# Performance work log

Hardware: AMD Instinct MI355X
Metric: run time of the kernel (lower is better)

Reference implementation:

```python
import jax, jax.numpy as jnp
import numpy as np

D_MODEL = 1024
N_HEADS = 16
HEAD_DIM = D_MODEL // N_HEADS


def _linear_params(key, fan_in, fan_out):
    kw, kb = jax.random.split(key)
    bound = 1.0 / np.sqrt(fan_in)
    W = jax.random.uniform(kw, (fan_in, fan_out), jnp.float32, -bound, bound)
    b = jax.random.uniform(kb, (fan_out,), jnp.float32, -bound, bound)
    return W, b


def setup_inputs() -> dict:
    key = jax.random.key(0)
    ks = jax.random.split(key, 7)
    B, N = 4, 2048
    q = jax.random.normal(ks[0], (B, N, D_MODEL), jnp.float32)
    k = jax.random.normal(ks[1], (B, N, D_MODEL), jnp.float32)
    v = jax.random.normal(ks[2], (B, N, D_MODEL), jnp.float32)
    Wq, bq = _linear_params(ks[3], D_MODEL, D_MODEL)
    Wk, bk = _linear_params(ks[4], D_MODEL, D_MODEL)
    Wv, bv = _linear_params(ks[5], D_MODEL, D_MODEL)
    Wo, bo = _linear_params(ks[6], D_MODEL, D_MODEL)
    return {"q": q, "k": k, "v": v,
            "Wq": Wq, "bq": bq, "Wk": Wk, "bk": bk,
            "Wv": Wv, "bv": bv, "Wo": Wo, "bo": bo}


def reference(q, k, v, Wq, bq, Wk, bk, Wv, bv, Wo, bo):
    B, N, _ = q.shape
    # fused QKV projection + head split: [B, N, D] -> [B, H, N, hd]
    def split_heads(x):
        return x.reshape(B, N, N_HEADS, HEAD_DIM).transpose(0, 2, 1, 3)
    qh = split_heads(q @ Wq + bq)
    kh = split_heads(k @ Wk + bk)
    vh = split_heads(v @ Wv + bv)
    # scaled dot-product attention (mask=None)
    scale = 1.0 / np.sqrt(HEAD_DIM)
    scores = jnp.einsum('bhqd,bhkd->bhqk', qh, kh) * scale  # [B,H,N,N]
    attn_weights = jax.nn.softmax(scores, axis=-1)
    attn_out = jnp.einsum('bhqk,bhkd->bhqd', attn_weights, vh)
    # merge heads: [B,H,N,hd] -> [B,N,D]
    attn_out = attn_out.transpose(0, 2, 1, 3).reshape(B, N, D_MODEL)
    output = attn_out @ Wo + bo
    return output, attn_weights
```

## Files before the change

### kernel.cpp

```cpp
#include <hip/hip_runtime.h>
#include <hip/hip_bf16.h>
#include <stdint.h>

#define D_MODEL 1024
#define NH      16
#define HD      64
#define B_SZ    4
#define SEQ     2048
#define M_TOT   (B_SZ*SEQ)
#define LOG2E_O8 0.18033688011112042f

typedef __bf16 bf16;
typedef bf16  bf16x8 __attribute__((ext_vector_type(8)));
typedef bf16  bf16x4 __attribute__((ext_vector_type(4)));
typedef float f32x4  __attribute__((ext_vector_type(4)));

static __device__ __forceinline__ f32x4 mfma16(bf16x8 a, bf16x8 b, f32x4 c) {
  return __builtin_amdgcn_mfma_f32_16x16x32_bf16(a, b, c, 0, 0, 0);
}

static __device__ __forceinline__ void gl2lds(const void* g, void* l) {
  __builtin_amdgcn_global_load_lds(
      (const __attribute__((address_space(1))) unsigned int*)g,
      (__attribute__((address_space(3))) unsigned int*)l,
      16, 0, 0);
}

#define BAR_VM16() do { \
  asm volatile("s_waitcnt vmcnt(16) lgkmcnt(0)" ::: "memory"); \
  __builtin_amdgcn_s_barrier(); \
  __builtin_amdgcn_sched_barrier(0); \
} while (0)

#define BAR_LGKM() do { \
  asm volatile("s_waitcnt lgkmcnt(0)" ::: "memory"); \
  __builtin_amdgcn_s_barrier(); \
  __builtin_amdgcn_sched_barrier(0); \
} while (0)

__global__ __launch_bounds__(256) void k_twt(const float* __restrict__ w0,
                                             const float* __restrict__ w1,
                                             const float* __restrict__ w2,
                                             const float* __restrict__ w3,
                                             bf16* __restrict__ t0,
                                             bf16* __restrict__ t1,
                                             bf16* __restrict__ t2,
                                             bf16* __restrict__ t3) {
  __shared__ bf16 t[64][65];
  int z = blockIdx.z;
  const float* W = z == 0 ? w0 : z == 1 ? w1 : z == 2 ? w2 : w3;
  bf16* Wt = z == 0 ? t0 : z == 1 ? t1 : z == 2 ? t2 : t3;
  int k0 = blockIdx.x * 64, n0 = blockIdx.y * 64;
  int r = threadIdx.x >> 2, c0 = (threadIdx.x & 3) * 16;
  const float* p = W + (size_t)(k0 + r) * D_MODEL + n0 + c0;
#pragma unroll
  for (int e = 0; e < 16; e += 4) {
    float4 v = *(const float4*)(p + e);
    t[r][c0+e+0] = (bf16)v.x; t[r][c0+e+1] = (bf16)v.y;
    t[r][c0+e+2] = (bf16)v.z; t[r][c0+e+3] = (bf16)v.w;
  }
  __syncthreads();
  bf16x8 o0, o1;
#pragma unroll
  for (int e = 0; e < 8; e++) { o0[e] = t[c0+e][r]; o1[e] = t[c0+8+e][r]; }
  bf16* q = Wt + (size_t)(n0 + r) * D_MODEL + k0 + c0;
  *(bf16x8*)q = o0; *(bf16x8*)(q + 8) = o1;
}

__global__ __launch_bounds__(256) void k_qkv(const float* __restrict__ Aq,
                                             const float* __restrict__ Ak,
                                             const float* __restrict__ Av,
                                             const bf16* __restrict__ Wt3,
                                             const float* __restrict__ bq,
                                             const float* __restrict__ bk,
                                             const float* __restrict__ bv,
                                             bf16* __restrict__ HQ,
                                             bf16* __restrict__ Vt) {
  __shared__ alignas(16) bf16 sA[2][8192];
  __shared__ alignas(16) bf16 sB[2][8192];
  const int tid = threadIdx.x;
  const int lane = tid & 63, wv = tid >> 6;
  const int g = lane >> 4, lr = lane & 15;
  const int wm = wv >> 1, wn = wv & 1;
  const int d = blockIdx.x;
  const int p = (d & 7) * 24 + (d >> 6);
  const int seg = p >> 6;
  const int m0 = (p & 63) * 128;
  const int n0 = ((d >> 3) & 7) * 128;

  const float* A = seg == 0 ? Aq : seg == 1 ? Ak : Av;
  const float* bias = seg == 0 ? bq : seg == 1 ? bk : bv;
  const float oscale = seg == 0 ? LOG2E_O8 : 1.0f;

  const float* ap[4]; int adst[4];
#pragma unroll
  for (int i = 0; i < 4; i++) {
    int row = i * 32 + (tid >> 3), col = (tid & 7) * 8;
    ap[i] = A + (size_t)(m0 + row) * D_MODEL + col;
    adst[i] = row * 128 + ((col * 2) ^ ((row & 7) << 4));
  }
  const char* bsrc[4]; int bdst[4];
#pragma unroll
  for (int i = 0; i < 4; i++) {
    int o = i * 4096 + tid * 16;
    int brow = o >> 7, bin = o & 127;
    bsrc[i] = (const char*)Wt3 + (size_t)(seg * 1024 + n0 + brow) * 2048
              + (bin ^ ((brow & 7) << 4));
    bdst[i] = i * 4096 + wv * 1024;
  }
  int fa[4], fb[4], swa[4], swb[4];
#pragma unroll
  for (int i = 0; i < 4; i++) {
    int rowa = wm * 64 + i * 16 + lr;
    int rowb = wn * 64 + i * 16 + lr;
    fa[i] = rowa * 128; swa[i] = (rowa & 7) << 4;
    fb[i] = rowb * 128; swb[i] = (rowb & 7) << 4;
  }
  f32x4 acc[4][4] = {};
  float4 af[4][2];

#pragma unroll
  for (int i = 0; i < 4; i++) gl2lds(bsrc[i], (char*)sB[0] + bdst[i]);
#pragma unroll
  for (int i = 0; i < 4; i++) { af[i][0] = *(const float4*)ap[i]; af[i][1] = *(const float4*)(ap[i] + 4); }
#pragma unroll
  for (int i = 0; i < 4; i++) {
    bf16x8 w8;
#pragma unroll
    for (int e = 0; e < 4; e++) { w8[e] = (bf16)af[i][0][e]; w8[4+e] = (bf16)af[i][1][e]; }
    *(bf16x8*)((char*)sA[0] + adst[i]) = w8;
  }
  __syncthreads();

  int cur = 0;
  for (int kt = 0; kt < 16; ++kt) {
    if (kt < 15) {
#pragma unroll
      for (int i = 0; i < 4; i++)
        gl2lds(bsrc[i] + (kt + 1) * 128, (char*)sB[cur ^ 1] + bdst[i]);
#pragma unroll
      for (int i = 0; i < 4; i++) {
        af[i][0] = *(const float4*)(ap[i] + (kt + 1) * 64);
        af[i][1] = *(const float4*)(ap[i] + (kt + 1) * 64 + 4);
      }
    }
    const char* bA = (const char*)sA[cur];
    const char* bB = (const char*)sB[cur];
#pragma unroll
    for (int c = 0; c < 2; c++) {
      bf16x8 a[4], b[4];
      int off = c * 64 + g * 16;
#pragma unroll
      for (int i = 0; i < 4; i++) {
        a[i] = *(const bf16x8*)(bA + fa[i] + (off ^ swa[i]));
        b[i] = *(const bf16x8*)(bB + fb[i] + (off ^ swb[i]));
      }
#pragma unroll
      for (int mi = 0; mi < 4; mi++)
#pragma unroll
        for (int ni = 0; ni < 4; ni++)
          acc[mi][ni] = mfma16(a[mi], b[ni], acc[mi][ni]);
    }
    if (kt < 15) {
#pragma unroll
      for (int i = 0; i < 4; i++) {
        bf16x8 w8;
#pragma unroll
        for (int e = 0; e < 4; e++) { w8[e] = (bf16)af[i][0][e]; w8[4+e] = (bf16)af[i][1][e]; }
        *(bf16x8*)((char*)sA[cur ^ 1] + adst[i]) = w8;
      }
    }
    __syncthreads();
    cur ^= 1;
  }

  if (seg < 2) {
    bf16* outp = HQ + (size_t)seg * 8388608;
#pragma unroll
    for (int mi = 0; mi < 4; mi++) {
#pragma unroll
      for (int ni = 0; ni < 4; ni++) {
        int n = n0 + wn * 64 + ni * 16 + lr;
        float bvl = bias[n];
        int h = n >> 6, dd = n & 63;
#pragma unroll
        for (int r = 0; r < 4; r++) {
          int m = m0 + wm * 64 + mi * 16 + g * 4 + r;
          int b = m >> 11, q = m & 2047;
          outp[(((size_t)(b * NH + h)) * SEQ + q) * HD + dd] =
              (bf16)((acc[mi][ni][r] + bvl) * oscale);
        }
      }
    }
  } else {
    char* tr = (char*)sA;
#pragma unroll
    for (int mi = 0; mi < 4; mi++) {
#pragma unroll
      for (int ni = 0; ni < 4; ni++) {
        int n_loc = wn * 64 + ni * 16 + lr;
        float bvl = bias[n0 + n_loc];
        bf16x4 pq;
#pragma unroll
        for (int r = 0; r < 4; r++) pq[r] = (bf16)(acc[mi][ni][r] + bvl);
        int m0l = wm * 64 + mi * 16 + g * 4;
        *(bf16x4*)(tr + n_loc * 256 + ((m0l * 2) ^ ((n_loc & 7) << 4))) = pq;
      }
    }
    __syncthreads();
    int n_loc = tid >> 1, mh = (tid & 1) * 64;
    int n_glob = n0 + n_loc;
    int h = n_glob >> 6, dd = n_glob & 63;
    int b = m0 >> 11, q0l = (m0 & 2047) + mh;
    bf16* vp = Vt + ((size_t)(b * NH + h) * HD + dd) * SEQ + q0l;
    int sw = (n_loc & 7) << 4;
#pragma unroll
    for (int c = 0; c < 8; c++) {
      bf16x8 v8 = *(const bf16x8*)(tr + n_loc * 256 + ((mh * 2 + c * 16) ^ sw));
      *(bf16x8*)(vp + c * 8) = v8;
    }
  }
}

__global__ __launch_bounds__(256) void k_ogemm(const bf16* __restrict__ A,
                                               const bf16* __restrict__ Bt,
                                               const float* __restrict__ bias,
                                               float* __restrict__ outp) {
  __shared__ alignas(16) bf16 sA[2][8192];
  __shared__ alignas(16) bf16 sB[2][8192];
  const int tid = threadIdx.x;
  const int lane = tid & 63, wv = tid >> 6;
  const int g = lane >> 4, lr = lane & 15;
  const int wm = wv >> 1, wn = wv & 1;
  const int d = blockIdx.x;
  const int m0 = ((d & 7) * 8 + (d >> 6)) * 128;
  const int n0 = ((d >> 3) & 7) * 128;

  const char* asrc[4]; const char* bsrc[4]; int dst[4];
#pragma unroll
  for (int i = 0; i < 4; i++) {
    int o = i * 4096 + tid * 16;
    int row = o >> 7, in = o & 127;
    int cs = in ^ ((row & 7) << 4);
    asrc[i] = (const char*)A  + (size_t)(m0 + row) * 2048 + cs;
    bsrc[i] = (const char*)Bt + (size_t)(n0 + row) * 2048 + cs;
    dst[i] = i * 4096 + wv * 1024;
  }
  int fa[4], fb[4], swa[4], swb[4];
#pragma unroll
  for (int i = 0; i < 4; i++) {
    int rowa = wm * 64 + i * 16 + lr;
    int rowb = wn * 64 + i * 16 + lr;
    fa[i] = rowa * 128; swa[i] = (rowa & 7) << 4;
    fb[i] = rowb * 128; swb[i] = (rowb & 7) << 4;
  }
  f32x4 acc[4][4] = {};
#pragma unroll
  for (int i = 0; i < 4; i++) {
    gl2lds(asrc[i], (char*)sA[0] + dst[i]);
    gl2lds(bsrc[i], (char*)sB[0] + dst[i]);
  }
  __syncthreads();
  int cur = 0;
  for (int kt = 0; kt < 16; ++kt) {
    if (kt < 15) {
#pragma unroll
      for (int i = 0; i < 4; i++) {
        gl2lds(asrc[i] + (kt + 1) * 128, (char*)sA[cur ^ 1] + dst[i]);
        gl2lds(bsrc[i] + (kt + 1) * 128, (char*)sB[cur ^ 1] + dst[i]);
      }
    }
    const char* bA = (const char*)sA[cur];
    const char* bB = (const char*)sB[cur];
#pragma unroll
    for (int c = 0; c < 2; c++) {
      bf16x8 a[4], b[4];
      int off = c * 64 + g * 16;
#pragma unroll
      for (int i = 0; i < 4; i++) {
        a[i] = *(const bf16x8*)(bA + fa[i] + (off ^ swa[i]));
        b[i] = *(const bf16x8*)(bB + fb[i] + (off ^ swb[i]));
      }
#pragma unroll
      for (int mi = 0; mi < 4; mi++)
#pragma unroll
        for (int ni = 0; ni < 4; ni++)
          acc[mi][ni] = mfma16(a[mi], b[ni], acc[mi][ni]);
    }
    __syncthreads();
    cur ^= 1;
  }
#pragma unroll
  for (int mi = 0; mi < 4; mi++) {
#pragma unroll
    for (int ni = 0; ni < 4; ni++) {
      int n = n0 + wn * 64 + ni * 16 + lr;
      float bvl = bias[n];
#pragma unroll
      for (int r = 0; r < 4; r++) {
        int m = m0 + wm * 64 + mi * 16 + g * 4 + r;
        outp[(size_t)m * D_MODEL + n] = acc[mi][ni][r] + bvl;
      }
    }
  }
}

__global__ __launch_bounds__(256) void k_attn(const bf16* __restrict__ Qh,
                                              const bf16* __restrict__ Kh,
                                              const bf16* __restrict__ Vt,
                                              float* __restrict__ Wout,
                                              bf16* __restrict__ O) {
  __shared__ alignas(16) bf16 sK[2][8192];
  __shared__ alignas(16) bf16 sV[8192];
  __shared__ alignas(16) bf16 sP[16384];
  const int tid = threadIdx.x, lane = tid & 63, wv = tid >> 6;
  const int g = lane >> 4, lr = lane & 15;
  int swzb = (blockIdx.x & 7) * 128 + (blockIdx.x >> 3);
  const int bh = swzb >> 4;
  const int qw = (swzb & 15) * 128 + wv * 32;

  bf16x8 qb[2][2];
#pragma unroll
  for (int mi = 0; mi < 2; mi++)
#pragma unroll
    for (int c = 0; c < 2; c++)
      qb[mi][c] = *(const bf16x8*)(Qh + ((size_t)bh * SEQ + qw + mi * 16 + lr) * HD + c * 32 + g * 8);

  const char* kbase = (const char*)(Kh + (size_t)bh * SEQ * HD);
  const char* vbase = (const char*)(Vt + (size_t)bh * HD * SEQ);
  const char* ksrc[4]; const char* vsrc[4]; int ldst[4];
#pragma unroll
  for (int i = 0; i < 4; i++) {
    int o = i * 4096 + tid * 16;
    int kr = o >> 7, kin = o & 127;
    ksrc[i] = kbase + (size_t)kr * 128 + (kin ^ ((kr & 7) << 4));
    int dr = o >> 8, vin = o & 255;
    vsrc[i] = vbase + (size_t)dr * 4096 + (vin ^ ((dr & 7) << 4));
    ldst[i] = i * 4096 + wv * 1024;
  }

#pragma unroll
  for (int i = 0; i < 4; i++) gl2lds(ksrc[i], (char*)sK + ldst[i]);
  __syncthreads();

  float rsum[2] = {0.f, 0.f};
  int cur = 0;
  for (int kt = 0; kt < 16; ++kt) {
    int nx = ((kt + 1) & 15) * 16384;
#pragma unroll
    for (int i = 0; i < 4; i++)
      gl2lds(ksrc[i] + nx, (char*)sK + (cur ^ 1) * 16384 + ldst[i]);
    const char* kb = (char*)sK + cur * 16384;
#pragma unroll
    for (int nf = 0; nf < 8; nf++) {
      int krow = nf * 16 + lr, sw = (krow & 7) << 4;
      bf16x8 k0 = *(const bf16x8*)(kb + krow * 128 + ((g * 16) ^ sw));
      bf16x8 k1 = *(const bf16x8*)(kb + krow * 128 + ((64 + g * 16) ^ sw));
#pragma unroll
      for (int mi = 0; mi < 2; mi++) {
        f32x4 t = {};
        t = mfma16(k0, qb[mi][0], t);
        t = mfma16(k1, qb[mi][1], t);
        rsum[mi] += __builtin_amdgcn_exp2f(t[0]) + __builtin_amdgcn_exp2f(t[1])
                  + __builtin_amdgcn_exp2f(t[2]) + __builtin_amdgcn_exp2f(t[3]);
      }
    }
    __syncthreads();
    cur ^= 1;
  }
  float lrl[2];
#pragma unroll
  for (int mi = 0; mi < 2; mi++) {
    float s = rsum[mi];
    s += __shfl_xor(s, 16); s += __shfl_xor(s, 32);
    lrl[mi] = -__builtin_amdgcn_logf(s);
  }
  const int osrc0 = (lane >> 3) + 16 * (lane & 3);
  const int osrc1 = 8 + (lane >> 3) + 16 * (lane & 3);
  const bool selhi = (lane >> 2) & 1;
  float* wrow[2][2];
#pragma unroll
  for (int mi = 0; mi < 2; mi++)
#pragma unroll
    for (int h = 0; h < 2; h++)
      wrow[mi][h] = Wout + ((size_t)bh * SEQ + qw + mi * 16 + 8 * h + (lane >> 3)) * SEQ
                    + 4 * (lane & 7);

  f32x4 oc[2][4] = {};
  for (int kt = 0; kt < 16; ++kt) {
#pragma unroll
    for (int i = 0; i < 4; i++) {
      if (kt < 15)
        gl2lds(ksrc[i] + (kt + 1) * 16384, (char*)sK + (cur ^ 1) * 16384 + ldst[i]);
      gl2lds(vsrc[i] + kt * 256, (char*)sV + ldst[i]);
    }
    const char* kb = (char*)sK + cur * 16384;
#pragma unroll
    for (int mi = 0; mi < 2; mi++) {
      f32x4 wreg[8];
#pragma unroll
      for (int nf = 0; nf < 8; nf++) {
        int krow = nf * 16 + lr, sw = (krow & 7) << 4;
        bf16x8 k0 = *(const bf16x8*)(kb + krow * 128 + ((g * 16) ^ sw));
        bf16x8 k1 = *(const bf16x8*)(kb + krow * 128 + ((64 + g * 16) ^ sw));
        f32x4 t = {};
        t = mfma16(k0, qb[mi][0], t);
        t = mfma16(k1, qb[mi][1], t);
        f32x4 w4;
        w4[0] = __builtin_amdgcn_exp2f(t[0] + lrl[mi]);
        w4[1] = __builtin_amdgcn_exp2f(t[1] + lrl[mi]);
        w4[2] = __builtin_amdgcn_exp2f(t[2] + lrl[mi]);
        w4[3] = __builtin_amdgcn_exp2f(t[3] + lrl[mi]);
        wreg[nf] = w4;
        bf16x4 p4;
        p4[0] = (bf16)w4[0]; p4[1] = (bf16)w4[1]; p4[2] = (bf16)w4[2]; p4[3] = (bf16)w4[3];
        int lq = wv * 32 + mi * 16 + lr;
        *(bf16x4*)((char*)sP + lq * 256 + (((nf * 16 + g * 4) * 2) ^ ((lq & 7) << 4))) = p4;
      }
#pragma unroll
      for (int h = 0; h < 2; h++) {
        int osrc = h ? osrc1 : osrc0;
#pragma unroll
        for (int c = 0; c < 4; c++) {
          f32x4 va, vb, outv;
#pragma unroll
          for (int e = 0; e < 4; e++) {
            va[e] = __shfl(wreg[2 * c][e], osrc);
            vb[e] = __shfl(wreg[2 * c + 1][e], osrc);
          }
#pragma unroll
          for (int e = 0; e < 4; e++) outv[e] = selhi ? vb[e] : va[e];
          __builtin_nontemporal_store(outv,
              (f32x4*)(wrow[mi][h] + kt * 128 + 32 * c));
        }
      }
    }
    BAR_VM16();
#pragma unroll
    for (int c = 0; c < 4; c++) {
      bf16x8 pa[2];
#pragma unroll
      for (int mi = 0; mi < 2; mi++) {
        int lq = wv * 32 + mi * 16 + lr;
        pa[mi] = *(const bf16x8*)((char*)sP + lq * 256 + ((c * 64 + g * 16) ^ ((lq & 7) << 4)));
      }
#pragma unroll
      for (int df = 0; df < 4; df++) {
        int dr = df * 16 + lr;
        bf16x8 vb2 = *(const bf16x8*)((char*)sV + dr * 256 + ((c * 64 + g * 16) ^ ((dr & 7) << 4)));
#pragma unroll
        for (int mi = 0; mi < 2; mi++)
          oc[mi][df] = mfma16(pa[mi], vb2, oc[mi][df]);
      }
    }
    BAR_LGKM();
    cur ^= 1;
  }
  int b = bh >> 4, h = bh & 15;
#pragma unroll
  for (int mi = 0; mi < 2; mi++)
#pragma unroll
    for (int df = 0; df < 4; df++)
#pragma unroll
      for (int r = 0; r < 4; r++) {
        int q = qw + mi * 16 + g * 4 + r;
        int dd = df * 16 + lr;
        O[((size_t)(b * SEQ + q) * NH + h) * HD + dd] = (bf16)oc[mi][df][r];
      }
}

extern "C" void kernel_launch(void* const* d_in, const int* in_sizes, int n_in,
                              void* d_out, int out_size, void* d_ws, size_t ws_size,
                              hipStream_t stream) {
  const float* q  = (const float*)d_in[0];
  const float* k  = (const float*)d_in[1];
  const float* v  = (const float*)d_in[2];
  const float* Wq = (const float*)d_in[3];
  const float* bq = (const float*)d_in[4];
  const float* Wk = (const float*)d_in[5];
  const float* bk = (const float*)d_in[6];
  const float* Wv = (const float*)d_in[7];
  const float* bv = (const float*)d_in[8];
  const float* Wo = (const float*)d_in[9];
  const float* bo = (const float*)d_in[10];

  char* ws = (char*)d_ws;
  bf16* Obuf = (bf16*)(ws);
  bf16* Wt3  = (bf16*)(ws + 16777216);
  bf16* WtO  = (bf16*)(ws + 16777216 + 3 * 2097152);
  bf16* HQ   = (bf16*)(ws + 25165824);
  bf16* Kh   = (bf16*)(ws + 41943040);
  bf16* Vt   = (bf16*)(ws + 75497472);

  float* out0 = (float*)d_out;
  float* wout = out0 + (size_t)M_TOT * D_MODEL;

  dim3 blk(256);
  k_twt<<<dim3(16, 16, 4), blk, 0, stream>>>(Wq, Wk, Wv, Wo,
                                             Wt3, Wt3 + 1048576, Wt3 + 2097152, WtO);
  k_qkv<<<dim3(1536), blk, 0, stream>>>(q, k, v, Wt3, bq, bk, bv, HQ, Vt);
  k_attn<<<dim3(1024), blk, 0, stream>>>(HQ, Kh, Vt, wout, Obuf);
  k_ogemm<<<dim3(512), blk, 0, stream>>>(Obuf, WtO, bo, out0);
}
```

Measured before the change: 372.4 us.

## Process two query tiles per attention block, fusing second tile's row-sum pass

Each attention block now handles 256 queries as two 128-query tiles, and the grid is halved. The row-sum (log-sum-exp) pass for the second tile runs inside the main weight/PV loop of the first tile, so K tiles loaded from LDS are reused. This removes one of the three K streaming passes per 256 queries. In exchange each block holds more registers (two sets of Q fragments and accumulators) and there are half as many blocks, which may reduce occupancy and parallelism.

Measured after the change: 372.9 us. Within noise of the previous version (+0.1%).

```diff
diff --git a/kernel.cpp b/kernel.cpp
--- a/kernel.cpp
+++ b/kernel.cpp
@@ -315,16 +315,20 @@
   __shared__ alignas(16) bf16 sP[16384];
   const int tid = threadIdx.x, lane = tid & 63, wv = tid >> 6;
   const int g = lane >> 4, lr = lane & 15;
-  int swzb = (blockIdx.x & 7) * 128 + (blockIdx.x >> 3);
-  const int bh = swzb >> 4;
-  const int qw = (swzb & 15) * 128 + wv * 32;
-
-  bf16x8 qb[2][2];
+  int swzb = (blockIdx.x & 7) * 64 + (blockIdx.x >> 3);
+  const int bh = swzb >> 3;
+  const int qt0 = (swzb & 7) * 256;
+  const int qw0 = qt0 + wv * 32;
+  const int qw1 = qt0 + 128 + wv * 32;
+
+  bf16x8 qb0[2][2], qb1[2][2];
 #pragma unroll
   for (int mi = 0; mi < 2; mi++)
 #pragma unroll
-    for (int c = 0; c < 2; c++)
-      qb[mi][c] = *(const bf16x8*)(Qh + ((size_t)bh * SEQ + qw + mi * 16 + lr) * HD + c * 32 + g * 8);
+    for (int c = 0; c < 2; c++) {
+      qb0[mi][c] = *(const bf16x8*)(Qh + ((size_t)bh * SEQ + qw0 + mi * 16 + lr) * HD + c * 32 + g * 8);
+      qb1[mi][c] = *(const bf16x8*)(Qh + ((size_t)bh * SEQ + qw1 + mi * 16 + lr) * HD + c * 32 + g * 8);
+    }
 
   const char* kbase = (const char*)(Kh + (size_t)bh * SEQ * HD);
   const char* vbase = (const char*)(Vt + (size_t)bh * HD * SEQ);
@@ -343,7 +347,7 @@
   for (int i = 0; i < 4; i++) gl2lds(ksrc[i], (char*)sK + ldst[i]);
   __syncthreads();
 
-  float rsum[2] = {0.f, 0.f};
+  float rsum0[2] = {0.f, 0.f};
   int cur = 0;
   for (int kt = 0; kt < 16; ++kt) {
     int nx = ((kt + 1) & 15) * 16384;
@@ -359,39 +363,42 @@
 #pragma unroll
       for (int mi = 0; mi < 2; mi++) {
         f32x4 t = {};
-        t = mfma16(k0, qb[mi][0], t);
-        t = mfma16(k1, qb[mi][1], t);
-        rsum[mi] += __builtin_amdgcn_exp2f(t[0]) + __builtin_amdgcn_exp2f(t[1])
-                  + __builtin_amdgcn_exp2f(t[2]) + __builtin_amdgcn_exp2f(t[3]);
+        t = mfma16(k0, qb0[mi][0], t);
+        t = mfma16(k1, qb0[mi][1], t);
+        rsum0[mi] += __builtin_amdgcn_exp2f(t[0]) + __builtin_amdgcn_exp2f(t[1])
+                   + __builtin_amdgcn_exp2f(t[2]) + __builtin_amdgcn_exp2f(t[3]);
       }
     }
     __syncthreads();
     cur ^= 1;
   }
-  float lrl[2];
+  float lrl0[2];
 #pragma unroll
   for (int mi = 0; mi < 2; mi++) {
-    float s = rsum[mi];
+    float s = rsum0[mi];
     s += __shfl_xor(s, 16); s += __shfl_xor(s, 32);
-    lrl[mi] = -__builtin_amdgcn_logf(s);
+    lrl0[mi] = -__builtin_amdgcn_logf(s);
   }
   const int osrc0 = (lane >> 3) + 16 * (lane & 3);
   const int osrc1 = 8 + (lane >> 3) + 16 * (lane & 3);
   const bool selhi = (lane >> 2) & 1;
-  float* wrow[2][2];
+  float* wrow0[2][2]; float* wrow1[2][2];
 #pragma unroll
   for (int mi = 0; mi < 2; mi++)
 #pragma unroll
-    for (int h = 0; h < 2; h++)
-      wrow[mi][h] = Wout + ((size_t)bh * SEQ + qw + mi * 16 + 8 * h + (lane >> 3)) * SEQ
-                    + 4 * (lane & 7);
-
-  f32x4 oc[2][4] = {};
+    for (int h = 0; h < 2; h++) {
+      wrow0[mi][h] = Wout + ((size_t)bh * SEQ + qw0 + mi * 16 + 8 * h + (lane >> 3)) * SEQ
+                     + 4 * (lane & 7);
+      wrow1[mi][h] = Wout + ((size_t)bh * SEQ + qw1 + mi * 16 + 8 * h + (lane >> 3)) * SEQ
+                     + 4 * (lane & 7);
+    }
+
+  float rsum1[2] = {0.f, 0.f};
+  f32x4 oc0[2][4] = {};
   for (int kt = 0; kt < 16; ++kt) {
 #pragma unroll
     for (int i = 0; i < 4; i++) {
-      if (kt < 15)
-        gl2lds(ksrc[i] + (kt + 1) * 16384, (char*)sK + (cur ^ 1) * 16384 + ldst[i]);
+      gl2lds(ksrc[i] + ((kt + 1) & 15) * 16384, (char*)sK + (cur ^ 1) * 16384 + ldst[i]);
       gl2lds(vsrc[i] + kt * 256, (char*)sV + ldst[i]);
     }
     const char* kb = (char*)sK + cur * 16384;
@@ -404,13 +411,13 @@
         bf16x8 k0 = *(const bf16x8*)(kb + krow * 128 + ((g * 16) ^ sw));
         bf16x8 k1 = *(const bf16x8*)(kb + krow * 128 + ((64 + g * 16) ^ sw));
         f32x4 t = {};
-        t = mfma16(k0, qb[mi][0], t);
-        t = mfma16(k1, qb[mi][1], t);
+        t = mfma16(k0, qb0[mi][0], t);
+        t = mfma16(k1, qb0[mi][1], t);
         f32x4 w4;
-        w4[0] = __builtin_amdgcn_exp2f(t[0] + lrl[mi]);
-        w4[1] = __builtin_amdgcn_exp2f(t[1] + lrl[mi]);
-        w4[2] = __builtin_amdgcn_exp2f(t[2] + lrl[mi]);
-        w4[3] = __builtin_amdgcn_exp2f(t[3] + lrl[mi]);
+        w4[0] = __builtin_amdgcn_exp2f(t[0] + lrl0[mi]);
+        w4[1] = __builtin_amdgcn_exp2f(t[1] + lrl0[mi]);
+        w4[2] = __builtin_amdgcn_exp2f(t[2] + lrl0[mi]);
+        w4[3] = __builtin_amdgcn_exp2f(t[3] + lrl0[mi]);
         wreg[nf] = w4;
         bf16x4 p4;
         p4[0] = (bf16)w4[0]; p4[1] = (bf16)w4[1]; p4[2] = (bf16)w4[2]; p4[3] = (bf16)w4[3];
@@ -431,8 +438,22 @@
 #pragma unroll
           for (int e = 0; e < 4; e++) outv[e] = selhi ? vb[e] : va[e];
           __builtin_nontemporal_store(outv,
-              (f32x4*)(wrow[mi][h] + kt * 128 + 32 * c));
+              (f32x4*)(wrow0[mi][h] + kt * 128 + 32 * c));
         }
+      }
+    }
+#pragma unroll
+    for (int nf = 0; nf < 8; nf++) {
+      int krow = nf * 16 + lr, sw = (krow & 7) << 4;
+      bf16x8 k0 = *(const bf16x8*)(kb + krow * 128 + ((g * 16) ^ sw));
+      bf16x8 k1 = *(const bf16x8*)(kb + krow * 128 + ((64 + g * 16) ^ sw));
+#pragma unroll
+      for (int mi = 0; mi < 2; mi++) {
+        f32x4 t = {};
+        t = mfma16(k0, qb1[mi][0], t);
+        t = mfma16(k1, qb1[mi][1], t);
+        rsum1[mi] += __builtin_amdgcn_exp2f(t[0]) + __builtin_amdgcn_exp2f(t[1])
+                   + __builtin_amdgcn_exp2f(t[2]) + __builtin_amdgcn_exp2f(t[3]);
       }
     }
     BAR_VM16();
@@ -450,23 +471,116 @@
         bf16x8 vb2 = *(const bf16x8*)((char*)sV + dr * 256 + ((c * 64 + g * 16) ^ ((dr & 7) << 4)));
 #pragma unroll
         for (int mi = 0; mi < 2; mi++)
-          oc[mi][df] = mfma16(pa[mi], vb2, oc[mi][df]);
+          oc0[mi][df] = mfma16(pa[mi], vb2, oc0[mi][df]);
       }
     }
     BAR_LGKM();
     cur ^= 1;
   }
-  int b = bh >> 4, h = bh & 15;
-#pragma unroll
-  for (int mi = 0; mi < 2; mi++)
-#pragma unroll
-    for (int df = 0; df < 4; df++)
-#pragma unroll
-      for (int r = 0; r < 4; r++) {
-        int q = qw + mi * 16 + g * 4 + r;
-        int dd = df * 16 + lr;
-        O[((size_t)(b * SEQ + q) * NH + h) * HD + dd] = (bf16)oc[mi][df][r];
-      }
+  float lrl1[2];
+#pragma unroll
+  for (int mi = 0; mi < 2; mi++) {
+    float s = rsum1[mi];
+    s += __shfl_xor(s, 16); s += __shfl_xor(s, 32);
+    lrl1[mi] = -__builtin_amdgcn_logf(s);
+  }
+  {
+    int b = bh >> 4, h = bh & 15;
+#pragma unroll
+    for (int mi = 0; mi < 2; mi++)
+#pragma unroll
+      for (int df = 0; df < 4; df++)
+#pragma unroll
+        for (int r = 0; r < 4; r++) {
+          int q = qw0 + mi * 16 + g * 4 + r;
+          int dd = df * 16 + lr;
+          O[((size_t)(b * SEQ + q) * NH + h) * HD + dd] = (bf16)oc0[mi][df][r];
+        }
+  }
+
+  f32x4 oc1[2][4] = {};
+  for (int kt = 0; kt < 16; ++kt) {
+#pragma unroll
+    for (int i = 0; i < 4; i++) {
+      if (kt < 15)
+        gl2lds(ksrc[i] + (kt + 1) * 16384, (char*)sK + (cur ^ 1) * 16384 + ldst[i]);
+      gl2lds(vsrc[i] + kt * 256, (char*)sV + ldst[i]);
+    }
+    const char* kb = (char*)sK + cur * 16384;
+#pragma unroll
+    for (int mi = 0; mi < 2; mi++) {
+      f32x4 wreg[8];
+#pragma unroll
+      for (int nf = 0; nf < 8; nf++) {
+        int krow = nf * 16 + lr, sw = (krow & 7) << 4;
+        bf16x8 k0 = *(const bf16x8*)(kb + krow * 128 + ((g * 16) ^ sw));
+        bf16x8 k1 = *(const bf16x8*)(kb + krow * 128 + ((64 + g * 16) ^ sw));
+        f32x4 t = {};
+        t = mfma16(k0, qb1[mi][0], t);
+        t = mfma16(k1, qb1[mi][1], t);
+        f32x4 w4;
+        w4[0] = __builtin_amdgcn_exp2f(t[0] + lrl1[mi]);
+        w4[1] = __builtin_amdgcn_exp2f(t[1] + lrl1[mi]);
+        w4[2] = __builtin_amdgcn_exp2f(t[2] + lrl1[mi]);
+        w4[3] = __builtin_amdgcn_exp2f(t[3] + lrl1[mi]);
+        wreg[nf] = w4;
+        bf16x4 p4;
+        p4[0] = (bf16)w4[0]; p4[1] = (bf16)w4[1]; p4[2] = (bf16)w4[2]; p4[3] = (bf16)w4[3];
+        int lq = wv * 32 + mi * 16 + lr;
+        *(bf16x4*)((char*)sP + lq * 256 + (((nf * 16 + g * 4) * 2) ^ ((lq & 7) << 4))) = p4;
+      }
+#pragma unroll
+      for (int h = 0; h < 2; h++) {
+        int osrc = h ? osrc1 : osrc0;
+#pragma unroll
+        for (int c = 0; c < 4; c++) {
+          f32x4 va, vb, outv;
+#pragma unroll
+          for (int e = 0; e < 4; e++) {
+            va[e] = __shfl(wreg[2 * c][e], osrc);
+            vb[e] = __shfl(wreg[2 * c + 1][e], osrc);
+          }
+#pragma unroll
+          for (int e = 0; e < 4; e++) outv[e] = selhi ? vb[e] : va[e];
+          __builtin_nontemporal_store(outv,
+              (f32x4*)(wrow1[mi][h] + kt * 128 + 32 * c));
+        }
+      }
+    }
+    BAR_VM16();
+#pragma unroll
+    for (int c = 0; c < 4; c++) {
+      bf16x8 pa[2];
+#pragma unroll
+      for (int mi = 0; mi < 2; mi++) {
+        int lq = wv * 32 + mi * 16 + lr;
+        pa[mi] = *(const bf16x8*)((char*)sP + lq * 256 + ((c * 64 + g * 16) ^ ((lq & 7) << 4)));
+      }
+#pragma unroll
+      for (int df = 0; df < 4; df++) {
+        int dr = df * 16 + lr;
+        bf16x8 vb2 = *(const bf16x8*)((char*)sV + dr * 256 + ((c * 64 + g * 16) ^ ((dr & 7) << 4)));
+#pragma unroll
+        for (int mi = 0; mi < 2; mi++)
+          oc1[mi][df] = mfma16(pa[mi], vb2, oc1[mi][df]);
+      }
+    }
+    BAR_LGKM();
+    cur ^= 1;
+  }
+  {
+    int b = bh >> 4, h = bh & 15;
+#pragma unroll
+    for (int mi = 0; mi < 2; mi++)
+#pragma unroll
+      for (int df = 0; df < 4; df++)
+#pragma unroll
+        for (int r = 0; r < 4; r++) {
+          int q = qw1 + mi * 16 + g * 4 + r;
+          int dd = df * 16 + lr;
+          O[((size_t)(b * SEQ + q) * NH + h) * HD + dd] = (bf16)oc1[mi][df][r];
+        }
+  }
 }
 
 extern "C" void kernel_launch(void* const* d_in, const int* in_sizes, int n_in,
@@ -499,6 +613,6 @@
   k_twt<<<dim3(16, 16, 4), blk, 0, stream>>>(Wq, Wk, Wv, Wo,
                                              Wt3, Wt3 + 1048576, Wt3 + 2097152, WtO);
   k_qkv<<<dim3(1536), blk, 0, stream>>>(q, k, v, Wt3, bq, bk, bv, HQ, Vt);
-  k_attn<<<dim3(1024), blk, 0, stream>>>(HQ, Kh, Vt, wout, Obuf);
+  k_attn<<<dim3(512), blk, 0, stream>>>(HQ, Kh, Vt, wout, Obuf);
   k_ogemm<<<dim3(512), blk, 0, stream>>>(Obuf, WtO, bo, out0);
 }
```

## Enlarge GEMM tiles to 128x256 with k32 stages and shrink attention K tiles

Applied to the files above, without the earlier changes.

The QKV and output-projection GEMMs now use 128x256 output tiles with a 32-wide K step, a new paired-row swizzled LDS layout, a triple-buffered A pipeline in the QKV kernel, and occupancy hints of two blocks per CU. The attention kernel processes 64-key tiles instead of 128, which shrinks its shared memory so more blocks can share a CU, and its wait counts are adjusted to match. The aim is more reuse per loaded tile and better latency hiding. In exchange, register pressure rises (32 accumulators per lane), there are twice as many barriers per K, and the grids are smaller, which can underfill the GPU.

New measurement: 357.4 us. 1.04x faster.

```diff
diff --git a/kernel.cpp b/kernel.cpp
--- a/kernel.cpp
+++ b/kernel.cpp
@@ -26,8 +26,8 @@
       16, 0, 0);
 }
 
-#define BAR_VM16() do { \
-  asm volatile("s_waitcnt vmcnt(16) lgkmcnt(0)" ::: "memory"); \
+#define BAR_VM8() do { \
+  asm volatile("s_waitcnt vmcnt(8) lgkmcnt(0)" ::: "memory"); \
   __builtin_amdgcn_s_barrier(); \
   __builtin_amdgcn_sched_barrier(0); \
 } while (0)
@@ -37,6 +37,10 @@
   __builtin_amdgcn_s_barrier(); \
   __builtin_amdgcn_sched_barrier(0); \
 } while (0)
+
+static __device__ __forceinline__ int lds_off(int r, int kb) {
+  return ((r >> 1) << 7) + ((((r & 1) << 6) + kb) ^ (((r >> 1) & 7) << 4));
+}
 
 __global__ __launch_bounds__(256) void k_twt(const float* __restrict__ w0,
                                              const float* __restrict__ w1,
@@ -67,111 +71,104 @@
   *(bf16x8*)q = o0; *(bf16x8*)(q + 8) = o1;
 }
 
-__global__ __launch_bounds__(256) void k_qkv(const float* __restrict__ Aq,
-                                             const float* __restrict__ Ak,
-                                             const float* __restrict__ Av,
-                                             const bf16* __restrict__ Wt3,
-                                             const float* __restrict__ bq,
-                                             const float* __restrict__ bk,
-                                             const float* __restrict__ bv,
-                                             bf16* __restrict__ HQ,
-                                             bf16* __restrict__ Vt) {
-  __shared__ alignas(16) bf16 sA[2][8192];
-  __shared__ alignas(16) bf16 sB[2][8192];
+__global__ __launch_bounds__(256, 2) void k_qkv8(const float* __restrict__ Aq,
+                                                 const float* __restrict__ Ak,
+                                                 const float* __restrict__ Av,
+                                                 const bf16* __restrict__ Wt3,
+                                                 const float* __restrict__ bq,
+                                                 const float* __restrict__ bk,
+                                                 const float* __restrict__ bv,
+                                                 bf16* __restrict__ HQ,
+                                                 bf16* __restrict__ Vt) {
+  __shared__ alignas(16) char smem[73728];
   const int tid = threadIdx.x;
   const int lane = tid & 63, wv = tid >> 6;
   const int g = lane >> 4, lr = lane & 15;
   const int wm = wv >> 1, wn = wv & 1;
-  const int d = blockIdx.x;
-  const int p = (d & 7) * 24 + (d >> 6);
-  const int seg = p >> 6;
-  const int m0 = (p & 63) * 128;
-  const int n0 = ((d >> 3) & 7) * 128;
+  const int dd = blockIdx.x;
+  const int P = (dd & 7) * 96 + (dd >> 3);
+  const int seg = P >> 8;
+  const int rem = P & 255;
+  const int m0 = (rem >> 2) * 128;
+  const int n0 = (rem & 3) * 256;
 
   const float* A = seg == 0 ? Aq : seg == 1 ? Ak : Av;
   const float* bias = seg == 0 ? bq : seg == 1 ? bk : bv;
   const float oscale = seg == 0 ? LOG2E_O8 : 1.0f;
 
-  const float* ap[4]; int adst[4];
-#pragma unroll
-  for (int i = 0; i < 4; i++) {
-    int row = i * 32 + (tid >> 3), col = (tid & 7) * 8;
-    ap[i] = A + (size_t)(m0 + row) * D_MODEL + col;
-    adst[i] = row * 128 + ((col * 2) ^ ((row & 7) << 4));
-  }
+  const float* aptr = A + (size_t)(m0 + (tid >> 1)) * D_MODEL + (tid & 1) * 16;
+  const int awoff0 = lds_off(tid >> 1, (tid & 1) * 32);
+  const int awoff1 = lds_off(tid >> 1, (tid & 1) * 32 + 16);
   const char* bsrc[4]; int bdst[4];
 #pragma unroll
-  for (int i = 0; i < 4; i++) {
-    int o = i * 4096 + tid * 16;
-    int brow = o >> 7, bin = o & 127;
-    bsrc[i] = (const char*)Wt3 + (size_t)(seg * 1024 + n0 + brow) * 2048
-              + (bin ^ ((brow & 7) << 4));
-    bdst[i] = i * 4096 + wv * 1024;
-  }
-  int fa[4], fb[4], swa[4], swb[4];
-#pragma unroll
-  for (int i = 0; i < 4; i++) {
-    int rowa = wm * 64 + i * 16 + lr;
-    int rowb = wn * 64 + i * 16 + lr;
-    fa[i] = rowa * 128; swa[i] = (rowa & 7) << 4;
-    fb[i] = rowb * 128; swb[i] = (rowb & 7) << 4;
-  }
-  f32x4 acc[4][4] = {};
-  float4 af[4][2];
-
-#pragma unroll
-  for (int i = 0; i < 4; i++) gl2lds(bsrc[i], (char*)sB[0] + bdst[i]);
-#pragma unroll
-  for (int i = 0; i < 4; i++) { af[i][0] = *(const float4*)ap[i]; af[i][1] = *(const float4*)(ap[i] + 4); }
-#pragma unroll
-  for (int i = 0; i < 4; i++) {
-    bf16x8 w8;
-#pragma unroll
-    for (int e = 0; e < 4; e++) { w8[e] = (bf16)af[i][0][e]; w8[4+e] = (bf16)af[i][1][e]; }
-    *(bf16x8*)((char*)sA[0] + adst[i]) = w8;
-  }
-  __syncthreads();
-
-  int cur = 0;
-  for (int kt = 0; kt < 16; ++kt) {
-    if (kt < 15) {
-#pragma unroll
-      for (int i = 0; i < 4; i++)
-        gl2lds(bsrc[i] + (kt + 1) * 128, (char*)sB[cur ^ 1] + bdst[i]);
-#pragma unroll
-      for (int i = 0; i < 4; i++) {
-        af[i][0] = *(const float4*)(ap[i] + (kt + 1) * 64);
-        af[i][1] = *(const float4*)(ap[i] + (kt + 1) * 64 + 4);
-      }
-    }
-    const char* bA = (const char*)sA[cur];
-    const char* bB = (const char*)sB[cur];
-#pragma unroll
-    for (int c = 0; c < 2; c++) {
-      bf16x8 a[4], b[4];
-      int off = c * 64 + g * 16;
-#pragma unroll
-      for (int i = 0; i < 4; i++) {
-        a[i] = *(const bf16x8*)(bA + fa[i] + (off ^ swa[i]));
-        b[i] = *(const bf16x8*)(bB + fb[i] + (off ^ swb[i]));
-      }
-#pragma unroll
-      for (int mi = 0; mi < 4; mi++)
-#pragma unroll
-        for (int ni = 0; ni < 4; ni++)
-          acc[mi][ni] = mfma16(a[mi], b[ni], acc[mi][ni]);
-    }
-    if (kt < 15) {
-#pragma unroll
-      for (int i = 0; i < 4; i++) {
-        bf16x8 w8;
-#pragma unroll
-        for (int e = 0; e < 4; e++) { w8[e] = (bf16)af[i][0][e]; w8[4+e] = (bf16)af[i][1][e]; }
-        *(bf16x8*)((char*)sA[cur ^ 1] + adst[i]) = w8;
-      }
-    }
-    __syncthreads();
-    cur ^= 1;
+  for (int u = 0; u < 4; u++) {
+    int o = u * 4096 + tid * 16;
+    int p = o >> 7, w = o & 127;
+    int wq = w ^ ((p & 7) << 4);
+    int r = p * 2 + (wq >> 6), kb = wq & 63;
+    bsrc[u] = (const char*)(Wt3 + (size_t)(seg * 1024 + n0 + r) * D_MODEL) + kb;
+    bdst[u] = o;
+  }
+  int aoff[4], boff[8];
+#pragma unroll
+  for (int mi = 0; mi < 4; mi++) aoff[mi] = lds_off(wm * 64 + mi * 16 + lr, g * 16);
+#pragma unroll
+  for (int ni = 0; ni < 8; ni++) boff[ni] = lds_off(wn * 128 + ni * 16 + lr, g * 16);
+
+  f32x4 acc[4][8] = {};
+  float4 af[4];
+
+#pragma unroll
+  for (int j = 0; j < 4; j++) af[j] = *(const float4*)(aptr + j * 4);
+#pragma unroll
+  for (int u = 0; u < 4; u++) gl2lds(bsrc[u], smem + 24576 + bdst[u]);
+  asm volatile("s_waitcnt vmcnt(0)" ::: "memory");
+  {
+    bf16x8 w8a, w8b;
+#pragma unroll
+    for (int e = 0; e < 4; e++) {
+      w8a[e] = (bf16)af[0][e]; w8a[4+e] = (bf16)af[1][e];
+      w8b[e] = (bf16)af[2][e]; w8b[4+e] = (bf16)af[3][e];
+    }
+    *(bf16x8*)(smem + awoff0) = w8a;
+    *(bf16x8*)(smem + awoff1) = w8b;
+  }
+
+  int bufc = 0;
+  for (int s = 0; s < 32; ++s) {
+    int kn = (s + 1) & 31;
+    int nxt = bufc + 1; if (nxt == 3) nxt = 0;
+#pragma unroll
+    for (int j = 0; j < 4; j++) af[j] = *(const float4*)(aptr + kn * 32 + j * 4);
+#pragma unroll
+    for (int u = 0; u < 4; u++)
+      gl2lds(bsrc[u] + kn * 64, smem + 24576 + nxt * 16384 + bdst[u]);
+    asm volatile("s_waitcnt vmcnt(8) lgkmcnt(0)" ::: "memory");
+    __builtin_amdgcn_s_barrier();
+    __builtin_amdgcn_sched_barrier(0);
+    const char* bA = smem + bufc * 8192;
+    const char* bB = smem + 24576 + bufc * 16384;
+    bf16x8 a[4], b[8];
+#pragma unroll
+    for (int mi = 0; mi < 4; mi++) a[mi] = *(const bf16x8*)(bA + aoff[mi]);
+#pragma unroll
+    for (int ni = 0; ni < 8; ni++) b[ni] = *(const bf16x8*)(bB + boff[ni]);
+#pragma unroll
+    for (int mi = 0; mi < 4; mi++)
+#pragma unroll
+      for (int ni = 0; ni < 8; ni++)
+        acc[mi][ni] = mfma16(a[mi], b[ni], acc[mi][ni]);
+    {
+      bf16x8 w8a, w8b;
+#pragma unroll
+      for (int e = 0; e < 4; e++) {
+        w8a[e] = (bf16)af[0][e]; w8a[4+e] = (bf16)af[1][e];
+        w8b[e] = (bf16)af[2][e]; w8b[4+e] = (bf16)af[3][e];
+      }
+      *(bf16x8*)(smem + nxt * 8192 + awoff0) = w8a;
+      *(bf16x8*)(smem + nxt * 8192 + awoff1) = w8b;
+    }
+    bufc = nxt;
   }
 
   if (seg < 2) {
@@ -179,26 +176,27 @@
 #pragma unroll
     for (int mi = 0; mi < 4; mi++) {
 #pragma unroll
-      for (int ni = 0; ni < 4; ni++) {
-        int n = n0 + wn * 64 + ni * 16 + lr;
+      for (int ni = 0; ni < 8; ni++) {
+        int n = n0 + wn * 128 + ni * 16 + lr;
         float bvl = bias[n];
-        int h = n >> 6, dd = n & 63;
+        int h = n >> 6, dcol = n & 63;
 #pragma unroll
         for (int r = 0; r < 4; r++) {
           int m = m0 + wm * 64 + mi * 16 + g * 4 + r;
-          int b = m >> 11, q = m & 2047;
-          outp[(((size_t)(b * NH + h)) * SEQ + q) * HD + dd] =
+          int b2 = m >> 11, q = m & 2047;
+          outp[(((size_t)(b2 * NH + h)) * SEQ + q) * HD + dcol] =
               (bf16)((acc[mi][ni][r] + bvl) * oscale);
         }
       }
     }
   } else {
-    char* tr = (char*)sA;
+    __syncthreads();
+    char* tr = smem;
 #pragma unroll
     for (int mi = 0; mi < 4; mi++) {
 #pragma unroll
-      for (int ni = 0; ni < 4; ni++) {
-        int n_loc = wn * 64 + ni * 16 + lr;
+      for (int ni = 0; ni < 8; ni++) {
+        int n_loc = wn * 128 + ni * 16 + lr;
         float bvl = bias[n0 + n_loc];
         bf16x4 pq;
 #pragma unroll
@@ -208,93 +206,99 @@
       }
     }
     __syncthreads();
-    int n_loc = tid >> 1, mh = (tid & 1) * 64;
+    int n_loc = tid;
     int n_glob = n0 + n_loc;
-    int h = n_glob >> 6, dd = n_glob & 63;
-    int b = m0 >> 11, q0l = (m0 & 2047) + mh;
-    bf16* vp = Vt + ((size_t)(b * NH + h) * HD + dd) * SEQ + q0l;
+    int h = n_glob >> 6, dcol = n_glob & 63;
+    int b2 = m0 >> 11, q0l = m0 & 2047;
+    bf16* vp = Vt + ((size_t)(b2 * NH + h) * HD + dcol) * SEQ + q0l;
     int sw = (n_loc & 7) << 4;
 #pragma unroll
-    for (int c = 0; c < 8; c++) {
-      bf16x8 v8 = *(const bf16x8*)(tr + n_loc * 256 + ((mh * 2 + c * 16) ^ sw));
+    for (int c = 0; c < 16; c++) {
+      bf16x8 v8 = *(const bf16x8*)(tr + n_loc * 256 + ((c * 16) ^ sw));
       *(bf16x8*)(vp + c * 8) = v8;
     }
   }
 }
 
-__global__ __launch_bounds__(256) void k_ogemm(const bf16* __restrict__ A,
-                                               const bf16* __restrict__ Bt,
-                                               const float* __restrict__ bias,
-                                               float* __restrict__ outp) {
-  __shared__ alignas(16) bf16 sA[2][8192];
-  __shared__ alignas(16) bf16 sB[2][8192];
+__global__ __launch_bounds__(256, 2) void k_ogemm8(const bf16* __restrict__ A,
+                                                   const bf16* __restrict__ Bt,
+                                                   const float* __restrict__ bias,
+                                                   float* __restrict__ outp) {
+  __shared__ alignas(16) char smem[49152];
   const int tid = threadIdx.x;
   const int lane = tid & 63, wv = tid >> 6;
   const int g = lane >> 4, lr = lane & 15;
   const int wm = wv >> 1, wn = wv & 1;
-  const int d = blockIdx.x;
-  const int m0 = ((d & 7) * 8 + (d >> 6)) * 128;
-  const int n0 = ((d >> 3) & 7) * 128;
-
-  const char* asrc[4]; const char* bsrc[4]; int dst[4];
-#pragma unroll
-  for (int i = 0; i < 4; i++) {
-    int o = i * 4096 + tid * 16;
-    int row = o >> 7, in = o & 127;
-    int cs = in ^ ((row & 7) << 4);
-    asrc[i] = (const char*)A  + (size_t)(m0 + row) * 2048 + cs;
-    bsrc[i] = (const char*)Bt + (size_t)(n0 + row) * 2048 + cs;
-    dst[i] = i * 4096 + wv * 1024;
-  }
-  int fa[4], fb[4], swa[4], swb[4];
-#pragma unroll
-  for (int i = 0; i < 4; i++) {
-    int rowa = wm * 64 + i * 16 + lr;
-    int rowb = wn * 64 + i * 16 + lr;
-    fa[i] = rowa * 128; swa[i] = (rowa & 7) << 4;
-    fb[i] = rowb * 128; swb[i] = (rowb & 7) << 4;
-  }
-  f32x4 acc[4][4] = {};
-#pragma unroll
-  for (int i = 0; i < 4; i++) {
-    gl2lds(asrc[i], (char*)sA[0] + dst[i]);
-    gl2lds(bsrc[i], (char*)sB[0] + dst[i]);
-  }
-  __syncthreads();
+  const int dd = blockIdx.x;
+  const int P = (dd & 7) * 32 + (dd >> 3);
+  const int m0 = (P >> 2) * 128;
+  const int n0 = (P & 3) * 256;
+
+  const char* asrc[2]; int adst[2];
+#pragma unroll
+  for (int u = 0; u < 2; u++) {
+    int o = u * 4096 + tid * 16;
+    int p = o >> 7, w = o & 127;
+    int wq = w ^ ((p & 7) << 4);
+    int r = p * 2 + (wq >> 6), kb = wq & 63;
+    asrc[u] = (const char*)(A + (size_t)(m0 + r) * D_MODEL) + kb;
+    adst[u] = o;
+  }
+  const char* bsrc[4]; int bdst[4];
+#pragma unroll
+  for (int u = 0; u < 4; u++) {
+    int o = u * 4096 + tid * 16;
+    int p = o >> 7, w = o & 127;
+    int wq = w ^ ((p & 7) << 4);
+    int r = p * 2 + (wq >> 6), kb = wq & 63;
+    bsrc[u] = (const char*)(Bt + (size_t)(n0 + r) * D_MODEL) + kb;
+    bdst[u] = o;
+  }
+  int aoff[4], boff[8];
+#pragma unroll
+  for (int mi = 0; mi < 4; mi++) aoff[mi] = lds_off(wm * 64 + mi * 16 + lr, g * 16);
+#pragma unroll
+  for (int ni = 0; ni < 8; ni++) boff[ni] = lds_off(wn * 128 + ni * 16 + lr, g * 16);
+
+  f32x4 acc[4][8] = {};
+#pragma unroll
+  for (int u = 0; u < 2; u++) gl2lds(asrc[u], smem + adst[u]);
+#pragma unroll
+  for (int u = 0; u < 4; u++) gl2lds(bsrc[u], smem + 16384 + bdst[u]);
+
   int cur = 0;
-  for (int kt = 0; kt < 16; ++kt) {
-    if (kt < 15) {
-#pragma unroll
-      for (int i = 0; i < 4; i++) {
-        gl2lds(asrc[i] + (kt + 1) * 128, (char*)sA[cur ^ 1] + dst[i]);
-        gl2lds(bsrc[i] + (kt + 1) * 128, (char*)sB[cur ^ 1] + dst[i]);
-      }
-    }
-    const char* bA = (const char*)sA[cur];
-    const char* bB = (const char*)sB[cur];
-#pragma unroll
-    for (int c = 0; c < 2; c++) {
-      bf16x8 a[4], b[4];
-      int off = c * 64 + g * 16;
-#pragma unroll
-      for (int i = 0; i < 4; i++) {
-        a[i] = *(const bf16x8*)(bA + fa[i] + (off ^ swa[i]));
-        b[i] = *(const bf16x8*)(bB + fb[i] + (off ^ swb[i]));
-      }
-#pragma unroll
-      for (int mi = 0; mi < 4; mi++)
-#pragma unroll
-        for (int ni = 0; ni < 4; ni++)
-          acc[mi][ni] = mfma16(a[mi], b[ni], acc[mi][ni]);
-    }
-    __syncthreads();
+  for (int s = 0; s < 32; ++s) {
+    int kn = (s + 1) & 31;
+#pragma unroll
+    for (int u = 0; u < 2; u++)
+      gl2lds(asrc[u] + kn * 64, smem + (cur ^ 1) * 8192 + adst[u]);
+#pragma unroll
+    for (int u = 0; u < 4; u++)
+      gl2lds(bsrc[u] + kn * 64, smem + 16384 + (cur ^ 1) * 16384 + bdst[u]);
+    asm volatile("s_waitcnt vmcnt(6)" ::: "memory");
+    __builtin_amdgcn_s_barrier();
+    __builtin_amdgcn_sched_barrier(0);
+    const char* bA = smem + cur * 8192;
+    const char* bB = smem + 16384 + cur * 16384;
+    bf16x8 a[4], b[8];
+#pragma unroll
+    for (int mi = 0; mi < 4; mi++) a[mi] = *(const bf16x8*)(bA + aoff[mi]);
+#pragma unroll
+    for (int ni = 0; ni < 8; ni++) b[ni] = *(const bf16x8*)(bB + boff[ni]);
+#pragma unroll
+    for (int mi = 0; mi < 4; mi++)
+#pragma unroll
+      for (int ni = 0; ni < 8; ni++)
+        acc[mi][ni] = mfma16(a[mi], b[ni], acc[mi][ni]);
+    asm volatile("s_waitcnt lgkmcnt(0)" ::: "memory");
+    __builtin_amdgcn_s_barrier();
     cur ^= 1;
   }
 #pragma unroll
   for (int mi = 0; mi < 4; mi++) {
 #pragma unroll
-    for (int ni = 0; ni < 4; ni++) {
-      int n = n0 + wn * 64 + ni * 16 + lr;
+    for (int ni = 0; ni < 8; ni++) {
+      int n = n0 + wn * 128 + ni * 16 + lr;
       float bvl = bias[n];
 #pragma unroll
       for (int r = 0; r < 4; r++) {
@@ -310,9 +314,7 @@
                                               const bf16* __restrict__ Vt,
                                               float* __restrict__ Wout,
                                               bf16* __restrict__ O) {
-  __shared__ alignas(16) bf16 sK[2][8192];
-  __shared__ alignas(16) bf16 sV[8192];
-  __shared__ alignas(16) bf16 sP[16384];
+  __shared__ alignas(16) char smem[40960];
   const int tid = threadIdx.x, lane = tid & 63, wv = tid >> 6;
   const int g = lane >> 4, lr = lane & 15;
   int swzb = (blockIdx.x & 7) * 128 + (blockIdx.x >> 3);
@@ -328,31 +330,32 @@
 
   const char* kbase = (const char*)(Kh + (size_t)bh * SEQ * HD);
   const char* vbase = (const char*)(Vt + (size_t)bh * HD * SEQ);
-  const char* ksrc[4]; const char* vsrc[4]; int ldst[4];
-#pragma unroll
-  for (int i = 0; i < 4; i++) {
+  const char* ksrc[2]; const char* vsrc[2]; int ldst[2];
+#pragma unroll
+  for (int i = 0; i < 2; i++) {
     int o = i * 4096 + tid * 16;
     int kr = o >> 7, kin = o & 127;
     ksrc[i] = kbase + (size_t)kr * 128 + (kin ^ ((kr & 7) << 4));
-    int dr = o >> 8, vin = o & 255;
+    int dr = o >> 7, vin = o & 127;
     vsrc[i] = vbase + (size_t)dr * 4096 + (vin ^ ((dr & 7) << 4));
-    ldst[i] = i * 4096 + wv * 1024;
-  }
-
-#pragma unroll
-  for (int i = 0; i < 4; i++) gl2lds(ksrc[i], (char*)sK + ldst[i]);
+    ldst[i] = i * 4096 + wv * 2048 + (tid & 63) * 16 - lane * 16 + lane * 16;
+    ldst[i] = o;
+  }
+
+#pragma unroll
+  for (int i = 0; i < 2; i++) gl2lds(ksrc[i], smem + ldst[i]);
   __syncthreads();
 
   float rsum[2] = {0.f, 0.f};
   int cur = 0;
-  for (int kt = 0; kt < 16; ++kt) {
-    int nx = ((kt + 1) & 15) * 16384;
-#pragma unroll
-    for (int i = 0; i < 4; i++)
-      gl2lds(ksrc[i] + nx, (char*)sK + (cur ^ 1) * 16384 + ldst[i]);
-    const char* kb = (char*)sK + cur * 16384;
-#pragma unroll
-    for (int nf = 0; nf < 8; nf++) {
+  for (int kt = 0; kt < 32; ++kt) {
+    int nx = ((kt + 1) & 31) * 8192;
+#pragma unroll
+    for (int i = 0; i < 2; i++)
+      gl2lds(ksrc[i] + nx, smem + (cur ^ 1) * 8192 + ldst[i]);
+    const char* kb = smem + cur * 8192;
+#pragma unroll
+    for (int nf = 0; nf < 4; nf++) {
       int krow = nf * 16 + lr, sw = (krow & 7) << 4;
       bf16x8 k0 = *(const bf16x8*)(kb + krow * 128 + ((g * 16) ^ sw));
       bf16x8 k1 = *(const bf16x8*)(kb + krow * 128 + ((64 + g * 16) ^ sw));
@@ -387,19 +390,18 @@
                     + 4 * (lane & 7);
 
   f32x4 oc[2][4] = {};
-  for (int kt = 0; kt < 16; ++kt) {
-#pragma unroll
-    for (int i = 0; i < 4; i++) {
-      if (kt < 15)
-        gl2lds(ksrc[i] + (kt + 1) * 16384, (char*)sK + (cur ^ 1) * 16384 + ldst[i]);
-      gl2lds(vsrc[i] + kt * 256, (char*)sV + ldst[i]);
-    }
-    const char* kb = (char*)sK + cur * 16384;
+  for (int kt = 0; kt < 32; ++kt) {
+#pragma unroll
+    for (int i = 0; i < 2; i++) {
+      gl2lds(ksrc[i] + ((kt + 1) & 31) * 8192, smem + (cur ^ 1) * 8192 + ldst[i]);
+      gl2lds(vsrc[i] + kt * 128, smem + 16384 + ldst[i]);
+    }
+    const char* kb = smem + cur * 8192;
 #pragma unroll
     for (int mi = 0; mi < 2; mi++) {
-      f32x4 wreg[8];
-#pragma unroll
-      for (int nf = 0; nf < 8; nf++) {
+      f32x4 wreg[4];
+#pragma unroll
+      for (int nf = 0; nf < 4; nf++) {
         int krow = nf * 16 + lr, sw = (krow & 7) << 4;
         bf16x8 k0 = *(const bf16x8*)(kb + krow * 128 + ((g * 16) ^ sw));
         bf16x8 k1 = *(const bf16x8*)(kb + krow * 128 + ((64 + g * 16) ^ sw));
@@ -415,13 +417,13 @@
         bf16x4 p4;
         p4[0] = (bf16)w4[0]; p4[1] = (bf16)w4[1]; p4[2] = (bf16)w4[2]; p4[3] = (bf16)w4[3];
         int lq = wv * 32 + mi * 16 + lr;
-        *(bf16x4*)((char*)sP + lq * 256 + (((nf * 16 + g * 4) * 2) ^ ((lq & 7) << 4))) = p4;
+        *(bf16x4*)(smem + 24576 + lq * 128 + (((nf * 16 + g * 4) * 2) ^ ((lq & 7) << 4))) = p4;
       }
 #pragma unroll
       for (int h = 0; h < 2; h++) {
         int osrc = h ? osrc1 : osrc0;
 #pragma unroll
-        for (int c = 0; c < 4; c++) {
+        for (int c = 0; c < 2; c++) {
           f32x4 va, vb, outv;
 #pragma unroll
           for (int e = 0; e < 4; e++) {
@@ -431,23 +433,23 @@
 #pragma unroll
           for (int e = 0; e < 4; e++) outv[e] = selhi ? vb[e] : va[e];
           __builtin_nontemporal_store(outv,
-              (f32x4*)(wrow[mi][h] + kt * 128 + 32 * c));
+              (f32x4*)(wrow[mi][h] + kt * 64 + 32 * c));
         }
       }
     }
-    BAR_VM16();
-#pragma unroll
-    for (int c = 0; c < 4; c++) {
+    BAR_VM8();
+#pragma unroll
+    for (int c = 0; c < 2; c++) {
       bf16x8 pa[2];
 #pragma unroll
       for (int mi = 0; mi < 2; mi++) {
         int lq = wv * 32 + mi * 16 + lr;
-        pa[mi] = *(const bf16x8*)((char*)sP + lq * 256 + ((c * 64 + g * 16) ^ ((lq & 7) << 4)));
+        pa[mi] = *(const bf16x8*)(smem + 24576 + lq * 128 + ((c * 64 + g * 16) ^ ((lq & 7) << 4)));
       }
 #pragma unroll
       for (int df = 0; df < 4; df++) {
         int dr = df * 16 + lr;
-        bf16x8 vb2 = *(const bf16x8*)((char*)sV + dr * 256 + ((c * 64 + g * 16) ^ ((dr & 7) << 4)));
+        bf16x8 vb2 = *(const bf16x8*)(smem + 16384 + dr * 128 + ((c * 64 + g * 16) ^ ((dr & 7) << 4)));
 #pragma unroll
         for (int mi = 0; mi < 2; mi++)
           oc[mi][df] = mfma16(pa[mi], vb2, oc[mi][df]);
@@ -464,8 +466,8 @@
 #pragma unroll
       for (int r = 0; r < 4; r++) {
         int q = qw + mi * 16 + g * 4 + r;
-        int dd = df * 16 + lr;
-        O[((size_t)(b * SEQ + q) * NH + h) * HD + dd] = (bf16)oc[mi][df][r];
+        int dcol = df * 16 + lr;
+        O[((size_t)(b * SEQ + q) * NH + h) * HD + dcol] = (bf16)oc[mi][df][r];
       }
 }
 
@@ -498,7 +500,7 @@
   dim3 blk(256);
   k_twt<<<dim3(16, 16, 4), blk, 0, stream>>>(Wq, Wk, Wv, Wo,
                                              Wt3, Wt3 + 1048576, Wt3 + 2097152, WtO);
-  k_qkv<<<dim3(1536), blk, 0, stream>>>(q, k, v, Wt3, bq, bk, bv, HQ, Vt);
+  k_qkv8<<<dim3(768), blk, 0, stream>>>(q, k, v, Wt3, bq, bk, bv, HQ, Vt);
   k_attn<<<dim3(1024), blk, 0, stream>>>(HQ, Kh, Vt, wout, Obuf);
-  k_ogemm<<<dim3(512), blk, 0, stream>>>(Obuf, WtO, bo, out0);
-}
+  k_ogemm8<<<dim3(256), blk, 0, stream>>>(Obuf, WtO, bo, out0);
+}
```
